# Kernel optimization log

Measured on AMD Instinct MI355X. Metric: run time of the kernel, lower is better.

The kernel has to match this reference:

```python
import jax, jax.numpy as jnp
import numpy as np

NUM_EMB = 256
EMB_DIM = 32
B, N = 16, 16384
TEMPERATURE = 1.0      # current value of the temperature buffer
TEMP_MIN = 0.5
TEMP_INIT_REF = 2.0    # constant used in temp_ratio denominator in the torch code


def setup_inputs() -> dict:
    key = jax.random.key(0)
    k1, k2, k3 = jax.random.split(key, 3)
    inputs = jax.random.normal(k1, (B, N, EMB_DIM), dtype=jnp.float32)
    embedding = jax.random.normal(k2, (NUM_EMB, EMB_DIM), dtype=jnp.float32) * 0.1
    gumbel_u = jax.random.uniform(k3, (B * N, NUM_EMB), dtype=jnp.float32)
    return {"inputs": inputs, "embedding": embedding, "gumbel_u": gumbel_u}


def reference(inputs, embedding, gumbel_u):
    input_shape = inputs.shape
    flat = inputs.reshape(-1, EMB_DIM)                       # [M, D]

    distances = (jnp.sum(flat ** 2, axis=1, keepdims=True)
                 - 2.0 * jnp.matmul(flat, embedding.T)
                 + jnp.sum(embedding ** 2, axis=1))
    logits = -distances / TEMPERATURE

    # training branch: gumbel noise + softmax at temperature
    gumbel = -jnp.log(-jnp.log(gumbel_u + 1e-20) + 1e-20)
    soft = jax.nn.softmax((logits + gumbel) / TEMPERATURE, axis=-1)  # [M, K]

    quantized_soft = jnp.matmul(soft, embedding)             # [M, D]
    indices = jnp.argmax(soft, axis=-1)                      # [M]
    quantized_hard = embedding[indices]                      # [M, D]

    temp_ratio = (TEMPERATURE - TEMP_MIN) / (TEMP_INIT_REF - TEMP_MIN)
    quantized = temp_ratio * quantized_soft + (1.0 - temp_ratio) * quantized_hard
    # straight-through estimator
    quantized = flat + jax.lax.stop_gradient(quantized - flat)

    commitment_loss = jnp.mean((jax.lax.stop_gradient(quantized_hard) - flat) ** 2)

    avg_probs = jnp.mean(soft, axis=0)                       # [K]
    perplexity = jnp.exp(-jnp.sum(avg_probs * jnp.log(avg_probs + 1e-10)))

    quantized = quantized.reshape(input_shape)
    indices = indices.reshape(input_shape[:-1])
    return quantized, commitment_loss, indices, perplexity
```

## Files before the change

kernel.cpp:

```cpp
#include <hip/hip_runtime.h>


#define M_ROWS  262144
#define OUT_LOSS 8388608
#define OUT_IDX  8388609
#define OUT_PPL  8650753

typedef float f32x2 __attribute__((ext_vector_type(2)));

__device__ __forceinline__ f32x2 mk2(float a, float b) {
  f32x2 r; r.x = a; r.y = b; return r;
}

__device__ __forceinline__ unsigned int f2bf_u(float f) {
  unsigned int u = __float_as_uint(f);
  u += 0x7fffu + ((u >> 16) & 1u);
  return u >> 16;
}
__device__ __forceinline__ float bf2f(unsigned int lo16) {
  return __uint_as_float(lo16 << 16);
}

__global__ __launch_bounds__(256) void vq_prep(const float* __restrict__ emb,
                                               float* __restrict__ ws) {
  int t = threadIdx.x;
  ws[t] = 0.0f;
  if (t == 0) ws[256] = 0.0f;
  const float4* e4 = (const float4*)emb;
  float s = 0.0f;
#pragma unroll
  for (int j = 0; j < 8; ++j) {
    float4 v = e4[t * 8 + j];
    s += v.x * v.x + v.y * v.y + v.z * v.z + v.w * v.w;
  }
  ws[257 + t] = s;
}

__global__ __launch_bounds__(256, 4) void vq_pass1(
    const float* __restrict__ x_in, const float* __restrict__ emb,
    const float* __restrict__ gum, const float* __restrict__ ne,
    float* __restrict__ invS_ws, unsigned short* __restrict__ p_ws,
    float* __restrict__ loss_ws, float* __restrict__ out) {
  __shared__ __align__(16) float x_lds[16 * 36];
  __shared__ __align__(16) float g_lds[16 * 256];
  __shared__ float t_lds[256 * 17];
  __shared__ float red_sum[16 * 17];
  __shared__ float red_max[16 * 17];
  __shared__ int   red_idx[16 * 17];

  const int tid = threadIdx.x;

  f32x2 er2[16];
  {
    const float4* e4 = (const float4*)(emb + tid * 32);
#pragma unroll
    for (int j = 0; j < 8; ++j) {
      float4 v = e4[j];
      er2[2*j]   = mk2(v.x, v.y);
      er2[2*j+1] = mk2(v.z, v.w);
    }
  }
  const float ne_t = ne[tid];
  const int row_blk = blockIdx.x * 256;
  float cl_acc = 0.0f;

  for (int tt = 0; tt < 16; ++tt) {
    const int r0 = row_blk + tt * 16;

    {
      const float4* gg = (const float4*)gum + (size_t)r0 * 64;
      float4* gd = (float4*)g_lds;
#pragma unroll
      for (int i = 0; i < 4; ++i) gd[i * 256 + tid] = gg[i * 256 + tid];
      if (tid < 128)
        *((float4*)&x_lds[(tid >> 3) * 36 + (tid & 7) * 4]) =
            ((const float4*)x_in)[(size_t)r0 * 8 + tid];
    }
    __syncthreads();

#pragma unroll 2
    for (int r = 0; r < 16; ++r) {
      const float4* xr4 = (const float4*)&x_lds[r * 36];
      f32x2 a0 = mk2(0.f, 0.f), a1 = mk2(0.f, 0.f);
#pragma unroll
      for (int j = 0; j < 8; ++j) {
        const float4 xv = xr4[j];
        a0 = __builtin_elementwise_fma(mk2(xv.x, xv.y), er2[2*j],   a0);
        a1 = __builtin_elementwise_fma(mk2(xv.z, xv.w), er2[2*j+1], a1);
      }
      const float dot = (a0.x + a1.x) + (a0.y + a1.y);
      const float u = g_lds[r * 256 + tid];
      const float g = -__logf(-__logf(u + 1e-20f) + 1e-20f);
      t_lds[tid * 17 + r] = fmaf(2.0f, dot, g) - ne_t;
    }
    __syncthreads();

    const int lrow = tid & 15;
    const int cs   = tid >> 4;
    {
      float ssum = 0.0f, tmax = -3.0e38f;
      int   kmax = 0;
      unsigned int packs[8];
#pragma unroll
      for (int j = 0; j < 16; ++j) {
        const int k = cs * 16 + j;
        const float tv = t_lds[k * 17 + lrow];
        const float p = __expf(tv);
        ssum += p;
        if (tv > tmax) { tmax = tv; kmax = k; }
        if (j & 1) packs[j >> 1] |= f2bf_u(p) << 16;
        else       packs[j >> 1]  = f2bf_u(p);
      }
      uint4* pout = (uint4*)(p_ws + (size_t)(r0 + lrow) * 256 + cs * 16);
      const uint4* pd = (const uint4*)packs;
      pout[0] = pd[0]; pout[1] = pd[1];
      red_sum[lrow * 17 + cs] = ssum;
      red_max[lrow * 17 + cs] = tmax;
      red_idx[lrow * 17 + cs] = kmax;
    }
    __syncthreads();

    if (tid < 16) {
      float ssum = 0.0f, tmax = -3.0e38f;
      int   kmax = 0;
#pragma unroll
      for (int c = 0; c < 16; ++c) {
        ssum += red_sum[tid * 17 + c];
        const float m = red_max[tid * 17 + c];
        if (m > tmax) { tmax = m; kmax = red_idx[tid * 17 + c]; }
      }
      const int rg = r0 + tid;
      invS_ws[rg] = 1.0f / ssum;
      out[OUT_IDX + rg] = (float)kmax;

      const float4* eh = (const float4*)(emb + (size_t)kmax * 32);
      const float* xrr = &x_lds[tid * 36];
      float cl = 0.0f;
#pragma unroll
      for (int j = 0; j < 8; ++j) {
        const float4 e  = eh[j];
        const float4 xv = ((const float4*)xrr)[j];
        float dx;
        dx = e.x - xv.x; cl = fmaf(dx, dx, cl);
        dx = e.y - xv.y; cl = fmaf(dx, dx, cl);
        dx = e.z - xv.z; cl = fmaf(dx, dx, cl);
        dx = e.w - xv.w; cl = fmaf(dx, dx, cl);
      }
#pragma unroll
      for (int off = 8; off > 0; off >>= 1) cl += __shfl_down(cl, off, 16);
      if (tid == 0) cl_acc += cl;
    }
    __syncthreads();
  }
  if (tid == 0) atomicAdd(loss_ws, cl_acc);
}

__global__ __launch_bounds__(256, 4) void vq_pass2(
    const float* __restrict__ emb, const unsigned short* __restrict__ p_ws,
    const float* __restrict__ invS_ws, float* __restrict__ out) {
  const int row = blockIdx.x * 256 + threadIdx.x;
  const float invS = invS_ws[row];
  const int imax = (int)out[OUT_IDX + row];
  const uint4* pv = (const uint4*)(p_ws + (size_t)row * 256);
  const float4* e4 = (const float4*)emb;

  f32x2 q2[16];
#pragma unroll
  for (int d = 0; d < 16; ++d) q2[d] = mk2(0.f, 0.f);

  for (int kg = 0; kg < 8; ++kg) {
    unsigned int w_[16];
#pragma unroll
    for (int j = 0; j < 4; ++j) {
      const uint4 v = pv[kg * 4 + j];
      w_[4*j+0] = v.x; w_[4*j+1] = v.y; w_[4*j+2] = v.z; w_[4*j+3] = v.w;
    }
#pragma unroll
    for (int i = 0; i < 16; ++i) {
      const int k0 = kg * 32 + 2 * i;
      const f32x2 pp0 = mk2(bf2f(w_[i] & 0xffffu), bf2f(w_[i] & 0xffffu));
      const f32x2 pp1 = mk2(bf2f(w_[i] >> 16),     bf2f(w_[i] >> 16));
#pragma unroll
      for (int jj = 0; jj < 8; ++jj) {
        const float4 e0 = e4[k0 * 8 + jj];
        const float4 e1 = e4[(k0 + 1) * 8 + jj];
        q2[2*jj]   = __builtin_elementwise_fma(mk2(e0.x, e0.y), pp0, q2[2*jj]);
        q2[2*jj+1] = __builtin_elementwise_fma(mk2(e0.z, e0.w), pp0, q2[2*jj+1]);
        q2[2*jj]   = __builtin_elementwise_fma(mk2(e1.x, e1.y), pp1, q2[2*jj]);
        q2[2*jj+1] = __builtin_elementwise_fma(mk2(e1.z, e1.w), pp1, q2[2*jj+1]);
      }
    }
  }

  const float tr  = 1.0f / 3.0f;
  const float otr = 1.0f - tr;
  const float4* ehv = (const float4*)(emb + (size_t)imax * 32);
  float4* outq = (float4*)(out + (size_t)row * 32);
#pragma unroll
  for (int j = 0; j < 8; ++j) {
    float4 e = ehv[j];
    float4 o;
    o.x = fmaf(tr, q2[2*j].x   * invS, otr * e.x);
    o.y = fmaf(tr, q2[2*j].y   * invS, otr * e.y);
    o.z = fmaf(tr, q2[2*j+1].x * invS, otr * e.z);
    o.w = fmaf(tr, q2[2*j+1].y * invS, otr * e.w);
    outq[j] = o;
  }
}

__global__ __launch_bounds__(256) void vq_avg(
    const unsigned short* __restrict__ p_ws, const float* __restrict__ invS_ws,
    float* __restrict__ avg_ws) {
  __shared__ float sh[256];
  const int tid = threadIdx.x, lane = tid & 63, w = tid >> 6;
  sh[tid] = 0.0f;
  __syncthreads();
  const int base = (blockIdx.x * 4 + w) * 32;
  const float iv = invS_ws[base + (lane & 31)];
  float a0 = 0.f, a1 = 0.f, a2 = 0.f, a3 = 0.f;
#pragma unroll 4
  for (int r = 0; r < 32; ++r) {
    const float s = __shfl(iv, r);
    const unsigned short* pr = p_ws + (size_t)(base + r) * 256;
    a0 = fmaf(bf2f(pr[  0 + lane]), s, a0);
    a1 = fmaf(bf2f(pr[ 64 + lane]), s, a1);
    a2 = fmaf(bf2f(pr[128 + lane]), s, a2);
    a3 = fmaf(bf2f(pr[192 + lane]), s, a3);
  }
  atomicAdd(&sh[  0 + lane], a0);
  atomicAdd(&sh[ 64 + lane], a1);
  atomicAdd(&sh[128 + lane], a2);
  atomicAdd(&sh[192 + lane], a3);
  __syncthreads();
  atomicAdd(&avg_ws[tid], sh[tid]);
}

__global__ __launch_bounds__(256) void vq_fin(const float* __restrict__ ws,
                                              float* __restrict__ out) {
  __shared__ float red[256];
  int t = threadIdx.x;
  float avg = ws[t] * (1.0f / 262144.0f);
  red[t] = -avg * __logf(avg + 1e-10f);
  __syncthreads();
  for (int s = 128; s > 0; s >>= 1) {
    if (t < s) red[t] += red[t + s];
    __syncthreads();
  }
  if (t == 0) {
    out[OUT_PPL]  = __expf(red[0]);
    out[OUT_LOSS] = ws[256] * (1.0f / 8388608.0f);
  }
}

__global__ __launch_bounds__(256, 1) void vq_main(
    const float* __restrict__ x_in, const float* __restrict__ emb,
    const float* __restrict__ gum, const float* __restrict__ ne,
    float* __restrict__ avg_ws, float* __restrict__ loss_ws,
    float* __restrict__ out) {
  extern __shared__ unsigned char dynsmem[];
  unsigned short* p_lds = (unsigned short*)dynsmem;

  const int tid  = threadIdx.x;
  const int lane = tid & 63;
  const int w    = tid >> 6;
  const int row  = blockIdx.x * 256 + tid;
  unsigned short* my_p = p_lds + (size_t)(w * 64 + lane) * 258;

  float xr[32];
  {
    const float4* xv = (const float4*)(x_in + (size_t)row * 32);
#pragma unroll
    for (int j = 0; j < 8; ++j) {
      float4 v = xv[j];
      xr[4*j+0] = v.x; xr[4*j+1] = v.y; xr[4*j+2] = v.z; xr[4*j+3] = v.w;
    }
  }
  float q[32];
#pragma unroll
  for (int d = 0; d < 32; ++d) q[d] = 0.0f;

  float ssum = 0.0f;
  float tmax = -3.0e38f;
  int   imax = 0;

  const float4* g4 = (const float4*)(gum + (size_t)row * 256);
  const float4* e4 = (const float4*)emb;

  for (int kg = 0; kg < 8; ++kg) {
    float uv[32];
#pragma unroll
    for (int j = 0; j < 8; ++j) {
      float4 v = g4[kg * 8 + j];
      uv[4*j+0] = v.x; uv[4*j+1] = v.y; uv[4*j+2] = v.z; uv[4*j+3] = v.w;
    }
#pragma unroll
    for (int kk = 0; kk < 32; ++kk) {
      const int k = kg * 32 + kk;
      float er[32];
#pragma unroll
      for (int j = 0; j < 8; ++j) {
        float4 v = e4[k * 8 + j];
        er[4*j+0] = v.x; er[4*j+1] = v.y; er[4*j+2] = v.z; er[4*j+3] = v.w;
      }
      float d0 = 0.f, d1 = 0.f, d2 = 0.f, d3 = 0.f;
#pragma unroll
      for (int d = 0; d < 32; d += 4) {
        d0 = fmaf(xr[d+0], er[d+0], d0);
        d1 = fmaf(xr[d+1], er[d+1], d1);
        d2 = fmaf(xr[d+2], er[d+2], d2);
        d3 = fmaf(xr[d+3], er[d+3], d3);
      }
      const float dot = (d0 + d1) + (d2 + d3);
      const float inner = -__logf(uv[kk] + 1e-20f);
      const float g = -__logf(inner + 1e-20f);
      const float t = fmaf(2.0f, dot, g) - ne[k];
      const float p = __expf(t);
      ssum += p;
      if (t > tmax) { tmax = t; imax = k; }
#pragma unroll
      for (int d = 0; d < 32; ++d) q[d] = fmaf(p, er[d], q[d]);
      my_p[k] = (unsigned short)f2bf_u(p);
    }
  }

  const float invS = 1.0f / ssum;
  {
    const float tr  = 1.0f / 3.0f;
    const float otr = 1.0f - tr;
    const float4* ehv = (const float4*)(emb + (size_t)imax * 32);
    float4* outq = (float4*)(out + (size_t)row * 32);
    float cl = 0.0f;
#pragma unroll
    for (int j = 0; j < 8; ++j) {
      float4 e = ehv[j];
      float4 o;
      float qs, dx;
      qs = q[4*j+0]*invS; o.x = tr*qs + otr*e.x; dx = e.x - xr[4*j+0]; cl = fmaf(dx,dx,cl);
      qs = q[4*j+1]*invS; o.y = tr*qs + otr*e.y; dx = e.y - xr[4*j+1]; cl = fmaf(dx,dx,cl);
      qs = q[4*j+2]*invS; o.z = tr*qs + otr*e.z; dx = e.z - xr[4*j+2]; cl = fmaf(dx,dx,cl);
      qs = q[4*j+3]*invS; o.w = tr*qs + otr*e.w; dx = e.w - xr[4*j+3]; cl = fmaf(dx,dx,cl);
      outq[j] = o;
    }
    out[OUT_IDX + row] = (float)imax;
#pragma unroll
    for (int off = 32; off > 0; off >>= 1) cl += __shfl_down(cl, off);
    if (lane == 0) atomicAdd(loss_ws, cl);
  }

  __syncthreads();

  float a0 = 0.f, a1 = 0.f, a2 = 0.f, a3 = 0.f;
  for (int r = 0; r < 64; ++r) {
    const float invS_r = __shfl(invS, r);
    const unsigned short* rp = p_lds + (size_t)(w * 64 + r) * 258;
    a0 = fmaf(bf2f(rp[  0 + lane]), invS_r, a0);
    a1 = fmaf(bf2f(rp[ 64 + lane]), invS_r, a1);
    a2 = fmaf(bf2f(rp[128 + lane]), invS_r, a2);
    a3 = fmaf(bf2f(rp[192 + lane]), invS_r, a3);
  }
  atomicAdd(&avg_ws[  0 + lane], a0);
  atomicAdd(&avg_ws[ 64 + lane], a1);
  atomicAdd(&avg_ws[128 + lane], a2);
  atomicAdd(&avg_ws[192 + lane], a3);
}

extern "C" void kernel_launch(void* const* d_in, const int* in_sizes, int n_in,
                              void* d_out, int out_size, void* d_ws, size_t ws_size,
                              hipStream_t stream) {
  const float* x   = (const float*)d_in[0];
  const float* emb = (const float*)d_in[1];
  const float* gum = (const float*)d_in[2];
  float* out = (float*)d_out;
  float* ws  = (float*)d_ws;

  (void)in_sizes; (void)n_in; (void)out_size;

  vq_prep<<<1, 256, 0, stream>>>(emb, ws);

  const size_t need = (size_t)(1024 + M_ROWS) * 4 + (size_t)M_ROWS * 256 * 2;
  if (ws_size >= need) {
    float* invS = ws + 1024;
    unsigned short* p = (unsigned short*)(ws + 1024 + M_ROWS);
    vq_pass1<<<1024, 256, 0, stream>>>(x, emb, gum, ws + 257, invS, p, ws + 256, out);
    vq_pass2<<<1024, 256, 0, stream>>>(emb, p, invS, out);
    vq_avg<<<2048, 256, 0, stream>>>(p, invS, ws);
  } else {
    hipFuncSetAttribute((const void*)vq_main,
                        hipFuncAttributeMaxDynamicSharedMemorySize, 132128);
    vq_main<<<1024, 256, 132128, stream>>>(x, emb, gum, ws + 257, ws, ws + 256, out);
  }
  vq_fin<<<1, 256, 0, stream>>>(ws, out);
}
```

Measured before the change: 317.1 us.

## Prefetch gumbel tiles via async global-to-LDS loads and stage codebook in LDS

In pass1, the gumbel noise tile for the next iteration is issued with global_load_lds right after the distance phase, so the load overlaps the softmax and reduction work instead of being a synchronous register round-trip at the top of each loop. In pass2, the 32KB codebook is copied into shared memory once per block and read from LDS instead of global/cache for every row. The prefetch depends on the builtin being available and on correct ordering with the later barriers. The pass2 LDS footprint may lower occupancy, and uniform-address LDS reads are broadcasts.

After: 319.0 us. No clear change (+0.6%).

```diff
diff --git a/kernel.cpp b/kernel.cpp
--- a/kernel.cpp
+++ b/kernel.cpp
@@ -5,6 +5,16 @@
 #define OUT_LOSS 8388608
 #define OUT_IDX  8388609
 #define OUT_PPL  8650753
+
+#if defined(__has_builtin)
+#if __has_builtin(__builtin_amdgcn_global_load_lds)
+#define HAVE_GLLDS 1
+#else
+#define HAVE_GLLDS 0
+#endif
+#else
+#define HAVE_GLLDS 0
+#endif
 
 typedef float f32x2 __attribute__((ext_vector_type(2)));
 
@@ -49,6 +59,8 @@
   __shared__ int   red_idx[16 * 17];
 
   const int tid = threadIdx.x;
+  const int wv  = tid >> 6;
+  const int ln  = tid & 63;
 
   f32x2 er2[16];
   {
@@ -64,18 +76,35 @@
   const int row_blk = blockIdx.x * 256;
   float cl_acc = 0.0f;
 
+#if HAVE_GLLDS
+  auto issue_g = [&](int ttn) {
+    const char* gbase = (const char*)(gum + (size_t)(row_blk + ttn * 16) * 256);
+#pragma unroll
+    for (int i = 0; i < 4; ++i) {
+      const int off = i * 4096 + wv * 1024;
+      __builtin_amdgcn_global_load_lds(
+          (const __attribute__((address_space(1))) void*)(gbase + off + ln * 16),
+          (__attribute__((address_space(3))) void*)((char*)g_lds + off),
+          16, 0, 0);
+    }
+  };
+  issue_g(0);
+#endif
+
   for (int tt = 0; tt < 16; ++tt) {
     const int r0 = row_blk + tt * 16;
 
+#if !HAVE_GLLDS
     {
       const float4* gg = (const float4*)gum + (size_t)r0 * 64;
       float4* gd = (float4*)g_lds;
 #pragma unroll
       for (int i = 0; i < 4; ++i) gd[i * 256 + tid] = gg[i * 256 + tid];
-      if (tid < 128)
-        *((float4*)&x_lds[(tid >> 3) * 36 + (tid & 7) * 4]) =
-            ((const float4*)x_in)[(size_t)r0 * 8 + tid];
-    }
+    }
+#endif
+    if (tid < 128)
+      *((float4*)&x_lds[(tid >> 3) * 36 + (tid & 7) * 4]) =
+          ((const float4*)x_in)[(size_t)r0 * 8 + tid];
     __syncthreads();
 
 #pragma unroll 2
@@ -94,6 +123,10 @@
       t_lds[tid * 17 + r] = fmaf(2.0f, dot, g) - ne_t;
     }
     __syncthreads();
+
+#if HAVE_GLLDS
+    if (tt < 15) issue_g(tt + 1);
+#endif
 
     const int lrow = tid & 15;
     const int cs   = tid >> 4;
@@ -158,11 +191,22 @@
 __global__ __launch_bounds__(256, 4) void vq_pass2(
     const float* __restrict__ emb, const unsigned short* __restrict__ p_ws,
     const float* __restrict__ invS_ws, float* __restrict__ out) {
-  const int row = blockIdx.x * 256 + threadIdx.x;
+  __shared__ __align__(16) float e_lds[256 * 32];
+
+  const int tid = threadIdx.x;
+  {
+    const float4* src = (const float4*)emb;
+    float4* dst = (float4*)e_lds;
+#pragma unroll
+    for (int j = 0; j < 8; ++j) dst[j * 256 + tid] = src[j * 256 + tid];
+  }
+  __syncthreads();
+
+  const int row = blockIdx.x * 256 + tid;
   const float invS = invS_ws[row];
   const int imax = (int)out[OUT_IDX + row];
   const uint4* pv = (const uint4*)(p_ws + (size_t)row * 256);
-  const float4* e4 = (const float4*)emb;
+  const float4* el4 = (const float4*)e_lds;
 
   f32x2 q2[16];
 #pragma unroll
@@ -182,8 +226,8 @@
       const f32x2 pp1 = mk2(bf2f(w_[i] >> 16),     bf2f(w_[i] >> 16));
 #pragma unroll
       for (int jj = 0; jj < 8; ++jj) {
-        const float4 e0 = e4[k0 * 8 + jj];
-        const float4 e1 = e4[(k0 + 1) * 8 + jj];
+        const float4 e0 = el4[k0 * 8 + jj];
+        const float4 e1 = el4[(k0 + 1) * 8 + jj];
         q2[2*jj]   = __builtin_elementwise_fma(mk2(e0.x, e0.y), pp0, q2[2*jj]);
         q2[2*jj+1] = __builtin_elementwise_fma(mk2(e0.z, e0.w), pp0, q2[2*jj+1]);
         q2[2*jj]   = __builtin_elementwise_fma(mk2(e1.x, e1.y), pp1, q2[2*jj]);
@@ -194,7 +238,7 @@
 
   const float tr  = 1.0f / 3.0f;
   const float otr = 1.0f - tr;
-  const float4* ehv = (const float4*)(emb + (size_t)imax * 32);
+  const float4* ehv = el4 + imax * 8;
   float4* outq = (float4*)(out + (size_t)row * 32);
 #pragma unroll
   for (int j = 0; j < 8; ++j) {
```
